# Optimization experiments

Hardware: AMD Instinct MI355X
Metric: run time of the kernel (lower is better)

Reference implementation:

```python
import jax, jax.numpy as jnp
from jax import lax
import numpy as np

B, L, D = 8, 2048, 512
Q, K = 8, 2048


def setup_inputs() -> dict:
    key = jax.random.key(0)
    kx, kc = jax.random.split(key)
    x = jax.random.normal(kx, (B, L, D), dtype=jnp.float32)
    codebooks = jax.random.normal(kc, (Q, K, D), dtype=jnp.float32)  # Q stacked [K, D] embedding tables
    return {"x": x, "codebooks": codebooks}


def reference(x, codebooks):
    # Residual VQ: at each level, nearest-codeword lookup on the residual.
    # cdist argmin == squared-distance argmin: ||r||^2 - 2 r.c + ||c||^2.
    cb_sq = jnp.sum(codebooks * codebooks, axis=-1)  # [Q, K]

    def step(residual, level):
        cb, cb2 = level  # [K, D], [K]
        r2 = jnp.sum(residual * residual, axis=-1, keepdims=True)  # [B, L, 1]
        dots = jnp.einsum('bld,kd->blk', residual, cb)  # [B, L, K]
        dist2 = r2 - 2.0 * dots + cb2  # [B, L, K]
        idx = jnp.argmin(dist2, axis=-1)  # [B, L]
        quant = cb[idx]  # [B, L, D] gather
        return residual - quant, (idx, quant)

    _, (indices, quants) = lax.scan(step, x, (codebooks, cb_sq))
    quantized = jnp.sum(quants, axis=0)  # [B, L, D]
    indices = jnp.moveaxis(indices, 0, 1)  # [B, Q, L] (torch.stack(dim=1))
    return indices, quantized
```

## Files before the change

### kernel.cpp

```cpp
#include <hip/hip_runtime.h>

#define BB 8
#define LL 2048
#define DD 512
#define QQ 8
#define KK 2048
#define MM (BB*LL)

#define NTILES 16

typedef __attribute__((ext_vector_type(8))) short short8;
typedef __attribute__((ext_vector_type(4))) float f32x4;

#define GLDS(src, dst) __builtin_amdgcn_global_load_lds( \
    (const __attribute__((address_space(1))) void*)(src), \
    (__attribute__((address_space(3))) void*)(dst), 16, 0, 0)

#define BARX()  asm volatile("s_barrier" ::: "memory")
#define WAIT0() asm volatile("s_waitcnt vmcnt(0)" ::: "memory")

__device__ __forceinline__ ushort f2bf(float f) {
    uint u = __float_as_uint(f);
    u += 0x7FFFu + ((u >> 16) & 1u);
    return (ushort)(u >> 16);
}

__global__ __launch_bounds__(256) void bprep_kernel(const float* __restrict__ cb,
                                                    short8* __restrict__ bh2all,
                                                    float* __restrict__ cb2) {
    const int wid  = threadIdx.x >> 6;
    const int lane = threadIdx.x & 63;
    const int col  = blockIdx.x * 4 + wid;
    const float* src = cb + (size_t)col * DD + lane * 8;
    float4 v0 = *(const float4*)src;
    float4 v1 = *(const float4*)(src + 4);
    short8 h;
    h[0] = (short)f2bf(v0.x); h[1] = (short)f2bf(v0.y);
    h[2] = (short)f2bf(v0.z); h[3] = (short)f2bf(v0.w);
    h[4] = (short)f2bf(v1.x); h[5] = (short)f2bf(v1.y);
    h[6] = (short)f2bf(v1.z); h[7] = (short)f2bf(v1.w);
    bh2all[(size_t)col * 64 + lane] = h;
    float s = v0.x*v0.x + v0.y*v0.y + v0.z*v0.z + v0.w*v0.w
            + v1.x*v1.x + v1.y*v1.y + v1.z*v1.z + v1.w*v1.w;
    #pragma unroll
    for (int off = 32; off >= 1; off >>= 1) s += __shfl_xor(s, off);
    if (lane == 0) cb2[col] = s;
}

__global__ __launch_bounds__(256) void aprep0_kernel(const float* __restrict__ x,
                                                     float* __restrict__ resid,
                                                     short8* __restrict__ ah) {
    const int wid  = threadIdx.x >> 6;
    const int lane = threadIdx.x & 63;
    const int row  = blockIdx.x * 4 + wid;
    const float* src = x + (size_t)row * DD + lane * 8;
    float4 v0 = *(const float4*)src;
    float4 v1 = *(const float4*)(src + 4);
    float* dst = resid + (size_t)row * DD + lane * 8;
    *(float4*)dst       = v0;
    *(float4*)(dst + 4) = v1;
    short8 h;
    h[0] = (short)f2bf(v0.x); h[1] = (short)f2bf(v0.y);
    h[2] = (short)f2bf(v0.z); h[3] = (short)f2bf(v0.w);
    h[4] = (short)f2bf(v1.x); h[5] = (short)f2bf(v1.y);
    h[6] = (short)f2bf(v1.z); h[7] = (short)f2bf(v1.w);
    ah[(size_t)row * 64 + lane] = h;
}

__global__ __launch_bounds__(512, 2) void gemm_argmin_kernel(
    const short8* __restrict__ ah,
    const short8* __restrict__ bh2q,
    const float*  __restrict__ cb2q,
    float*        __restrict__ blockv1,
    uint4*        __restrict__ blockmask,
    float W)
{
    __shared__ char smemc[131072];

    const int id  = blockIdx.x;
    const int xcd = id & 7;
    const int s   = id >> 3;
    const int nt  = s & 7;
    const int mt  = xcd * 8 + (s >> 3);

    const int tid  = threadIdx.x;
    const int wid  = tid >> 6;
    const int lane = tid & 63;
    const int wr   = wid >> 2;
    const int wcn  = wid & 3;
    const int l15  = lane & 15, l4 = lane >> 4;

    f32x4 acc[4][8];
    #pragma unroll
    for (int n = 0; n < 4; n++)
        #pragma unroll
        for (int m = 0; m < 8; m++) acc[n][m] = (f32x4){0.f, 0.f, 0.f, 0.f};

    const char* aSrc = (const char*)ah   + ((size_t)mt << 18);
    const char* bSrc = (const char*)bh2q + ((size_t)nt << 18);

    #define STAGEQ(tt, bufn, p) do { \
        int g_ = (p) * 512 + tid; \
        int rL_ = g_ >> 3, st_ = g_ & 7; \
        int k_ = st_ ^ (rL_ & 7); \
        char* db_ = smemc + (bufn) * 65536 + ((p) * 512 + wid * 64) * 16; \
        GLDS(aSrc + (size_t)rL_ * 1024 + (tt) * 128 + k_ * 16, db_); \
        GLDS(bSrc + (size_t)rL_ * 1024 + (tt) * 128 + k_ * 16, db_ + 32768); \
    } while (0)

    short8 af[4][2], bf[4][2];

    #define LDA(mh) do { \
        _Pragma("unroll") for (int mm = 0; mm < 4; mm++) \
        _Pragma("unroll") for (int ks = 0; ks < 2; ks++) { \
            int rL_ = wr * 128 + ((mh) * 4 + mm) * 16 + l15; \
            int c_ = ks * 4 + l4; \
            af[mm][ks] = *(const short8*)(smemc + ab + rL_ * 128 + ((c_ ^ (rL_ & 7)) << 4)); \
        } } while (0)

    #define LDBALL() do { \
        _Pragma("unroll") for (int nn = 0; nn < 4; nn++) \
        _Pragma("unroll") for (int ks = 0; ks < 2; ks++) { \
            int cL_ = wcn * 64 + nn * 16 + l15; \
            int c_ = ks * 4 + l4; \
            bf[nn][ks] = *(const short8*)(smemc + ab + 32768 + cL_ * 128 + ((c_ ^ (cL_ & 7)) << 4)); \
        } } while (0)

    #define PH(mh) do { \
        __builtin_amdgcn_s_setprio(1); \
        _Pragma("unroll") for (int ks = 0; ks < 2; ks++) \
        _Pragma("unroll") for (int nn = 0; nn < 4; nn++) \
        _Pragma("unroll") for (int mm = 0; mm < 4; mm++) \
            acc[nn][(mh)*4+mm] = __builtin_amdgcn_mfma_f32_16x16x32_bf16( \
                bf[nn][ks], af[mm][ks], acc[nn][(mh)*4+mm], 0, 0, 0); \
        __builtin_amdgcn_s_setprio(0); \
    } while (0)

    STAGEQ(0, 0, 0); STAGEQ(0, 0, 1); STAGEQ(0, 0, 2); STAGEQ(0, 0, 3);
    WAIT0();
    BARX();

    for (int t = 0; t < 8; t++) {
        const uint ab = (uint)(t & 1) * 65536u;
        const int nbuf = (t & 1) ^ 1;
        if (t < 7) { STAGEQ(t + 1, nbuf, 0); STAGEQ(t + 1, nbuf, 1);
                     STAGEQ(t + 1, nbuf, 2); STAGEQ(t + 1, nbuf, 3); }
        LDBALL();
        LDA(0);
        PH(0);
        LDA(1);
        PH(1);
        if (t < 7) WAIT0();
        BARX();
    }

    float* halfmin = (float*)smemc;
    uint2* maskS   = (uint2*)(smemc + 4096);

    f32x4 c2v[4];
    #pragma unroll
    for (int n = 0; n < 4; n++)
        c2v[n] = *(const f32x4*)&cb2q[nt * 256 + wcn * 64 + n * 16 + (l4 << 2)];

    #pragma unroll
    for (int m = 0; m < 8; m++) {
        float v = 3.4e38f;
        #pragma unroll
        for (int n = 0; n < 4; n++)
            #pragma unroll
            for (int r = 0; r < 4; r++)
                v = fminf(v, fmaf(-2.f, acc[n][m][r], c2v[n][r]));
        v = fminf(v, __shfl_xor(v, 16));
        v = fminf(v, __shfl_xor(v, 32));
        if (l4 == 0) halfmin[(wr * 128 + m * 16 + l15) * 4 + wcn] = v;
    }
    __syncthreads();

    #pragma unroll
    for (int m = 0; m < 8; m++) {
        int rL = wr * 128 + m * 16 + l15;
        int pb = wcn & 2;
        float vt = fminf(halfmin[rL * 4 + pb], halfmin[rL * 4 + pb + 1]);
        float thrm = vt + W;
        uint blo = 0, bhi = 0;
        #pragma unroll
        for (int n = 0; n < 4; n++)
            #pragma unroll
            for (int r = 0; r < 4; r++) {
                float d = fmaf(-2.f, acc[n][m][r], c2v[n][r]);
                int bit = n * 16 + (l4 << 2) + r;
                if (d < thrm) { if (bit < 32) blo |= 1u << bit; else bhi |= 1u << (bit - 32); }
            }
        blo |= __shfl_xor(blo, 16); bhi |= __shfl_xor(bhi, 16);
        blo |= __shfl_xor(blo, 32); bhi |= __shfl_xor(bhi, 32);
        if (l4 == 0) maskS[rL * 4 + wcn] = make_uint2(blo, bhi);
    }
    __syncthreads();

    {
        int T = tid >> 8, rL = tid & 255;
        float vt = fminf(halfmin[rL * 4 + T * 2], halfmin[rL * 4 + T * 2 + 1]);
        uint2 lo = maskS[rL * 4 + T * 2], hi = maskS[rL * 4 + T * 2 + 1];
        size_t o = (size_t)(nt * 2 + T) * MM + mt * 256 + rL;
        blockv1[o] = vt;
        blockmask[o] = make_uint4(lo.x, lo.y, hi.x, hi.y);
    }
    #undef STAGEQ
    #undef LDA
    #undef LDBALL
    #undef PH
}

__global__ __launch_bounds__(256) void crru_kernel(
    const float*  __restrict__ blockv1,
    const uint4*  __restrict__ blockmask,
    const float*  __restrict__ cbq,
    const float*  __restrict__ cb2q,
    const float*  __restrict__ xin,
    float*        __restrict__ resid,
    float*        __restrict__ idx_out,
    short8*       __restrict__ ah,
    int q, float W)
{
    __shared__ float rs[4][DD];
    const int wid  = threadIdx.x >> 6;
    const int lane = threadIdx.x & 63;
    const int row  = blockIdx.x * 4 + wid;
    const int grp  = lane >> 4, gl = lane & 15;

    float v1 = 3.4e38f;
    uint4 mk = make_uint4(0, 0, 0, 0);
    if (lane < NTILES) {
        size_t o = (size_t)lane * MM + row;
        v1 = blockv1[o];
        mk = blockmask[o];
    }

    float* rrow = resid + (size_t)row * DD + lane * 8;
    float4 r0 = *(const float4*)rrow;
    float4 r1 = *(const float4*)(rrow + 4);
    *(float4*)&rs[wid][lane * 8]     = r0;
    *(float4*)&rs[wid][lane * 8 + 4] = r1;

    float g1 = v1;
    #pragma unroll
    for (int off = 32; off >= 1; off >>= 1) g1 = fminf(g1, __shfl_xor(g1, off));
    const float thr = g1 + W;

    unsigned long long act = __ballot((lane < NTILES) && (v1 < thr));

    float be = 3.4e38f; int bk = 0x7FFFFFFF;
    const float* rsw = rs[wid];

    auto eval4 = [&](int k0, int k1, int k2, int k3) {
        int kg = (grp == 0) ? k0 : (grp == 1) ? k1 : (grp == 2) ? k2 : k3;
        float d = 0.f;
        if (kg >= 0) {
            const float* cp = cbq + (size_t)kg * DD + gl * 32;
            const float* rp = rsw + gl * 32;
            #pragma unroll
            for (int j = 0; j < 8; j++) {
                float4 c = *(const float4*)(cp + j * 4);
                float4 r = *(const float4*)(rp + j * 4);
                d = fmaf(r.x, c.x, d); d = fmaf(r.y, c.y, d);
                d = fmaf(r.z, c.z, d); d = fmaf(r.w, c.w, d);
            }
        }
        #pragma unroll
        for (int off = 8; off >= 1; off >>= 1) d += __shfl_xor(d, off);
        #pragma unroll
        for (int g = 0; g < 4; g++) {
            float dg = __shfl(d, g * 16);
            int kg2 = (g == 0) ? k0 : (g == 1) ? k1 : (g == 2) ? k2 : k3;
            if (kg2 >= 0) {
                float e = fmaf(-2.f, dg, cb2q[kg2]);
                if (e < be || (e == be && kg2 < bk)) { be = e; bk = kg2; }
            }
        }
    };

    while (act) {
        int tile = __ffsll(act) - 1; act &= act - 1;
        uint m0 = __shfl((int)mk.x, tile), m1 = __shfl((int)mk.y, tile);
        uint m2 = __shfl((int)mk.z, tile), m3 = __shfl((int)mk.w, tile);
        unsigned long long lo = ((unsigned long long)m1 << 32) | m0;
        unsigned long long hi = ((unsigned long long)m3 << 32) | m2;
        int base = tile * 128;
        while (lo | hi) {
            int c0 = -1, c1 = -1, c2 = -1, c3 = -1;
            #define POP1(dst) \
                if (lo) { int b = __ffsll(lo) - 1; lo &= lo - 1; dst = base + b; } \
                else if (hi) { int b = __ffsll(hi) - 1; hi &= hi - 1; dst = base + 64 + b; }
            POP1(c0) POP1(c1) POP1(c2) POP1(c3)
            #undef POP1
            eval4(c0, c1, c2, c3);
        }
    }
    const int winner = bk;

    if (lane == 0) {
        int b = row >> 11, l = row & (LL - 1);
        idx_out[((size_t)b * QQ + q) * LL + l] = (float)winner;
    }

    const float* cw = cbq + (size_t)winner * DD + lane * 8;
    float4 c0 = *(const float4*)cw;
    float4 c1 = *(const float4*)(cw + 4);
    float4 n0 = make_float4(r0.x - c0.x, r0.y - c0.y, r0.z - c0.z, r0.w - c0.w);
    float4 n1 = make_float4(r1.x - c1.x, r1.y - c1.y, r1.z - c1.z, r1.w - c1.w);

    if (q < QQ - 1) {
        *(float4*)rrow       = n0;
        *(float4*)(rrow + 4) = n1;
        short8 h;
        h[0] = (short)f2bf(n0.x); h[1] = (short)f2bf(n0.y);
        h[2] = (short)f2bf(n0.z); h[3] = (short)f2bf(n0.w);
        h[4] = (short)f2bf(n1.x); h[5] = (short)f2bf(n1.y);
        h[6] = (short)f2bf(n1.z); h[7] = (short)f2bf(n1.w);
        ah[(size_t)row * 64 + lane] = h;
    } else {
        const float* xw = xin + (size_t)row * DD + lane * 8;
        float4 x0 = *(const float4*)xw;
        float4 x1 = *(const float4*)(xw + 4);
        *(float4*)rrow       = make_float4(x0.x - n0.x, x0.y - n0.y, x0.z - n0.z, x0.w - n0.w);
        *(float4*)(rrow + 4) = make_float4(x1.x - n1.x, x1.y - n1.y, x1.z - n1.z, x1.w - n1.w);
    }
}

extern "C" void kernel_launch(void* const* d_in, const int* in_sizes, int n_in,
                              void* d_out, int out_size, void* d_ws, size_t ws_size,
                              hipStream_t stream) {
    (void)in_sizes; (void)n_in; (void)out_size; (void)ws_size;
    const float* x  = (const float*)d_in[0];
    const float* cb = (const float*)d_in[1];
    float* out = (float*)d_out;

    float* idx_out = out;
    float* resid   = out + (size_t)BB * QQ * LL;

    char* w = (char*)d_ws;
    float*  cb2       = (float*)(w);
    float*  blockv1   = (float*)(w + 0x10000);
    uint4*  blockmask = (uint4*)(w + 0x110000);
    short8* ah        = (short8*)(w + 0x510000);
    short8* bh2all    = (short8*)(w + 0x1510000);

    bprep_kernel<<<QQ * KK / 4, 256, 0, stream>>>(cb, bh2all, cb2);
    aprep0_kernel<<<MM / 4, 256, 0, stream>>>(x, resid, ah);

    for (int q = 0; q < QQ; q++) {
        const float* cbq  = cb + (size_t)q * KK * DD;
        const float* c2q  = cb2 + (size_t)q * KK;
        const short8* bhq = bh2all + (size_t)q * KK * 64;
        const float W = 2.0f + 0.3f * q;

        gemm_argmin_kernel<<<512, 512, 0, stream>>>(ah, bhq, c2q,
                                                    blockv1, blockmask, W);

        crru_kernel<<<MM / 4, 256, 0, stream>>>(blockv1, blockmask, cbq, c2q, x,
                                                resid, idx_out, ah, q, W);
    }
}
```

Measured before the change: 500.1 us.

## Split GEMM K-tile into half-stages with partial vmcnt waits and interleaved A/B LDS layout

The bf16 MFMA distance GEMM now stages each K-tile in two halves, each holding interleaved A and B rows under a new swizzle, instead of four quarter-copies of A and B. The main loop waits with vmcnt(4) rather than draining all loads. Barriers move so the copy of the next tile's half starts right after the current half is consumed. The aim is to overlap global-to-LDS copies with MFMA work at finer grain and remove full vmcnt(0) stalls, at the cost of more barriers per tile and a more complex swizzle that must stay correct.

```diff
diff --git a/kernel.cpp b/kernel.cpp
--- a/kernel.cpp
+++ b/kernel.cpp
@@ -16,8 +16,9 @@
     (const __attribute__((address_space(1))) void*)(src), \
     (__attribute__((address_space(3))) void*)(dst), 16, 0, 0)
 
-#define BARX()  asm volatile("s_barrier" ::: "memory")
-#define WAIT0() asm volatile("s_waitcnt vmcnt(0)" ::: "memory")
+#define BARX()   asm volatile("s_barrier" ::: "memory")
+#define WAIT0()  asm volatile("s_waitcnt vmcnt(0)" ::: "memory")
+#define WAITV4() asm volatile("s_waitcnt vmcnt(4)" ::: "memory")
 
 __device__ __forceinline__ ushort f2bf(float f) {
     uint u = __float_as_uint(f);
@@ -99,59 +100,57 @@
     const char* aSrc = (const char*)ah   + ((size_t)mt << 18);
     const char* bSrc = (const char*)bh2q + ((size_t)nt << 18);
 
-    #define STAGEQ(tt, bufn, p) do { \
-        int g_ = (p) * 512 + tid; \
-        int rL_ = g_ >> 3, st_ = g_ & 7; \
-        int k_ = st_ ^ (rL_ & 7); \
-        char* db_ = smemc + (bufn) * 65536 + ((p) * 512 + wid * 64) * 16; \
-        GLDS(aSrc + (size_t)rL_ * 1024 + (tt) * 128 + k_ * 16, db_); \
-        GLDS(bSrc + (size_t)rL_ * 1024 + (tt) * 128 + k_ * 16, db_ + 32768); \
-    } while (0)
-
-    short8 af[4][2], bf[4][2];
-
-    #define LDA(mh) do { \
-        _Pragma("unroll") for (int mm = 0; mm < 4; mm++) \
-        _Pragma("unroll") for (int ks = 0; ks < 2; ks++) { \
-            int rL_ = wr * 128 + ((mh) * 4 + mm) * 16 + l15; \
-            int c_ = ks * 4 + l4; \
-            af[mm][ks] = *(const short8*)(smemc + ab + rL_ * 128 + ((c_ ^ (rL_ & 7)) << 4)); \
+    #define STAGEH(tt, bufn, h) do { \
+        _Pragma("unroll") for (int j = 0; j < 4; j++) { \
+            int g_  = wid * 4 + j; \
+            int pr_ = g_ * 8 + (lane >> 3); \
+            int isB_ = ((lane >> 2) & 1) ^ ((pr_ >> 2) & 1); \
+            int sl_  = (lane & 3) ^ (pr_ & 3); \
+            const char* s_ = (isB_ ? bSrc : aSrc) + (size_t)pr_ * 1024 \
+                             + (tt) * 128 + ((h) * 4 + sl_) * 16; \
+            GLDS(s_, smemc + (bufn) * 65536 + (h) * 32768 + g_ * 1024); \
         } } while (0)
 
-    #define LDBALL() do { \
+    short8 af[8], bf[4];
+
+    #define LDAB(ks) do { \
+        _Pragma("unroll") for (int mm = 0; mm < 8; mm++) { \
+            int rL_ = wr * 128 + mm * 16 + l15; \
+            af[mm] = *(const short8*)(smemc + ab + (ks) * 32768 + rL_ * 128 \
+                     + (((rL_ >> 2) & 1) << 6) + ((l4 ^ (rL_ & 3)) << 4)); \
+        } \
+        _Pragma("unroll") for (int nn = 0; nn < 4; nn++) { \
+            int cL_ = wcn * 64 + nn * 16 + l15; \
+            bf[nn] = *(const short8*)(smemc + ab + (ks) * 32768 + cL_ * 128 \
+                     + ((1 ^ ((cL_ >> 2) & 1)) << 6) + ((l4 ^ (cL_ & 3)) << 4)); \
+        } } while (0)
+
+    #define PHALL() do { \
+        __builtin_amdgcn_s_setprio(1); \
         _Pragma("unroll") for (int nn = 0; nn < 4; nn++) \
-        _Pragma("unroll") for (int ks = 0; ks < 2; ks++) { \
-            int cL_ = wcn * 64 + nn * 16 + l15; \
-            int c_ = ks * 4 + l4; \
-            bf[nn][ks] = *(const short8*)(smemc + ab + 32768 + cL_ * 128 + ((c_ ^ (cL_ & 7)) << 4)); \
-        } } while (0)
-
-    #define PH(mh) do { \
-        __builtin_amdgcn_s_setprio(1); \
-        _Pragma("unroll") for (int ks = 0; ks < 2; ks++) \
-        _Pragma("unroll") for (int nn = 0; nn < 4; nn++) \
-        _Pragma("unroll") for (int mm = 0; mm < 4; mm++) \
-            acc[nn][(mh)*4+mm] = __builtin_amdgcn_mfma_f32_16x16x32_bf16( \
-                bf[nn][ks], af[mm][ks], acc[nn][(mh)*4+mm], 0, 0, 0); \
+        _Pragma("unroll") for (int mm = 0; mm < 8; mm++) \
+            acc[nn][mm] = __builtin_amdgcn_mfma_f32_16x16x32_bf16( \
+                bf[nn], af[mm], acc[nn][mm], 0, 0, 0); \
         __builtin_amdgcn_s_setprio(0); \
     } while (0)
 
-    STAGEQ(0, 0, 0); STAGEQ(0, 0, 1); STAGEQ(0, 0, 2); STAGEQ(0, 0, 3);
-    WAIT0();
-    BARX();
-
+    STAGEH(0, 0, 0);
+    STAGEH(0, 0, 1);
+
+    #pragma unroll
     for (int t = 0; t < 8; t++) {
         const uint ab = (uint)(t & 1) * 65536u;
         const int nbuf = (t & 1) ^ 1;
-        if (t < 7) { STAGEQ(t + 1, nbuf, 0); STAGEQ(t + 1, nbuf, 1);
-                     STAGEQ(t + 1, nbuf, 2); STAGEQ(t + 1, nbuf, 3); }
-        LDBALL();
-        LDA(0);
-        PH(0);
-        LDA(1);
-        PH(1);
-        if (t < 7) WAIT0();
+        WAITV4();
         BARX();
+        if (t < 7) STAGEH(t + 1, nbuf, 0);
+        LDAB(0);
+        PHALL();
+        if (t < 7) { WAITV4(); } else { WAIT0(); }
+        BARX();
+        if (t < 7) STAGEH(t + 1, nbuf, 1);
+        LDAB(1);
+        PHALL();
     }
 
     float* halfmin = (float*)smemc;
@@ -205,10 +204,9 @@
         blockv1[o] = vt;
         blockmask[o] = make_uint4(lo.x, lo.y, hi.x, hi.y);
     }
-    #undef STAGEQ
-    #undef LDA
-    #undef LDBALL
-    #undef PH
+    #undef STAGEH
+    #undef LDAB
+    #undef PHALL
 }
 
 __global__ __launch_bounds__(256) void crru_kernel(
```

New measurement: 504.7 us. Within noise of the previous version (+0.9%).

## Split GEMM tile loads into quarter stages with partial vmcnt waits

Applied to the files above, without the earlier changes.

The bf16 MFMA distance GEMM loop is restructured from whole-tile double buffering with a full vmcnt(0) wait per k-step into four quarter-tile stages. Each stage covers A or B rows for one half of the wave's subtile. Compute on each quarter starts after only its own data has landed (vmcnt(4)/vmcnt(2)) and loads for the next k-tile are issued in between, so global-to-LDS traffic overlaps more with MFMA work. The cost is more barriers per iteration, harder index math for the staging, and the risk of getting the wait-count or buffer ordering wrong.

```diff
diff --git a/kernel.cpp b/kernel.cpp
--- a/kernel.cpp
+++ b/kernel.cpp
@@ -16,8 +16,10 @@
     (const __attribute__((address_space(1))) void*)(src), \
     (__attribute__((address_space(3))) void*)(dst), 16, 0, 0)
 
-#define BARX()  asm volatile("s_barrier" ::: "memory")
-#define WAIT0() asm volatile("s_waitcnt vmcnt(0)" ::: "memory")
+#define BARX()   asm volatile("s_barrier" ::: "memory")
+#define WAIT0()  asm volatile("s_waitcnt vmcnt(0)" ::: "memory")
+#define WAITV2() asm volatile("s_waitcnt vmcnt(2)" ::: "memory")
+#define WAITV4() asm volatile("s_waitcnt vmcnt(4)" ::: "memory")
 
 __device__ __forceinline__ ushort f2bf(float f) {
     uint u = __float_as_uint(f);
@@ -99,14 +101,20 @@
     const char* aSrc = (const char*)ah   + ((size_t)mt << 18);
     const char* bSrc = (const char*)bh2q + ((size_t)nt << 18);
 
-    #define STAGEQ(tt, bufn, p) do { \
-        int g_ = (p) * 512 + tid; \
-        int rL_ = g_ >> 3, st_ = g_ & 7; \
-        int k_ = st_ ^ (rL_ & 7); \
-        char* db_ = smemc + (bufn) * 65536 + ((p) * 512 + wid * 64) * 16; \
-        GLDS(aSrc + (size_t)rL_ * 1024 + (tt) * 128 + k_ * 16, db_); \
-        GLDS(bSrc + (size_t)rL_ * 1024 + (tt) * 128 + k_ * 16, db_ + 32768); \
-    } while (0)
+    #define STAGEU(tt, bufn, isB, u) do { \
+        _Pragma("unroll") for (int j = 0; j < 2; j++) { \
+            int riu0 = j * 64 + wid * 8;                 \
+            int riu  = riu0 + (lane >> 3); \
+            int st   = lane & 7; \
+            int rc  = (isB) ? (((riu  >> 5) << 6) + (u) * 32 + (riu  & 31)) \
+                            : (((riu  >> 6) << 7) + (u) * 64 + (riu  & 63)); \
+            int rc0 = (isB) ? (((riu0 >> 5) << 6) + (u) * 32 + (riu0 & 31)) \
+                            : (((riu0 >> 6) << 7) + (u) * 64 + (riu0 & 63)); \
+            int k_ = st ^ (rc & 7); \
+            const char* s_ = ((isB) ? bSrc : aSrc) + (size_t)rc * 1024 \
+                             + (tt) * 128 + k_ * 16; \
+            GLDS(s_, smemc + (bufn) * 65536 + ((isB) ? 32768 : 0) + rc0 * 128); \
+        } } while (0)
 
     short8 af[4][2], bf[4][2];
 
@@ -118,40 +126,60 @@
             af[mm][ks] = *(const short8*)(smemc + ab + rL_ * 128 + ((c_ ^ (rL_ & 7)) << 4)); \
         } } while (0)
 
-    #define LDBALL() do { \
-        _Pragma("unroll") for (int nn = 0; nn < 4; nn++) \
+    #define LDB2(nh) do { \
+        _Pragma("unroll") for (int n2 = 0; n2 < 2; n2++) \
         _Pragma("unroll") for (int ks = 0; ks < 2; ks++) { \
+            int nn = (nh) * 2 + n2; \
             int cL_ = wcn * 64 + nn * 16 + l15; \
             int c_ = ks * 4 + l4; \
             bf[nn][ks] = *(const short8*)(smemc + ab + 32768 + cL_ * 128 + ((c_ ^ (cL_ & 7)) << 4)); \
         } } while (0)
 
-    #define PH(mh) do { \
+    #define PHQ(mh, nh) do { \
         __builtin_amdgcn_s_setprio(1); \
         _Pragma("unroll") for (int ks = 0; ks < 2; ks++) \
-        _Pragma("unroll") for (int nn = 0; nn < 4; nn++) \
+        _Pragma("unroll") for (int n2 = 0; n2 < 2; n2++) \
         _Pragma("unroll") for (int mm = 0; mm < 4; mm++) \
-            acc[nn][(mh)*4+mm] = __builtin_amdgcn_mfma_f32_16x16x32_bf16( \
-                bf[nn][ks], af[mm][ks], acc[nn][(mh)*4+mm], 0, 0, 0); \
+            acc[(nh)*2+n2][(mh)*4+mm] = __builtin_amdgcn_mfma_f32_16x16x32_bf16( \
+                bf[(nh)*2+n2][ks], af[mm][ks], acc[(nh)*2+n2][(mh)*4+mm], 0, 0, 0); \
         __builtin_amdgcn_s_setprio(0); \
     } while (0)
 
-    STAGEQ(0, 0, 0); STAGEQ(0, 0, 1); STAGEQ(0, 0, 2); STAGEQ(0, 0, 3);
-    WAIT0();
-    BARX();
-
-    for (int t = 0; t < 8; t++) {
+    STAGEU(0, 0, 0, 0);
+    STAGEU(0, 0, 1, 0);
+    STAGEU(0, 0, 1, 1);
+    STAGEU(0, 0, 0, 1);
+
+    for (int t = 0; t < 7; t++) {
         const uint ab = (uint)(t & 1) * 65536u;
         const int nbuf = (t & 1) ^ 1;
-        if (t < 7) { STAGEQ(t + 1, nbuf, 0); STAGEQ(t + 1, nbuf, 1);
-                     STAGEQ(t + 1, nbuf, 2); STAGEQ(t + 1, nbuf, 3); }
-        LDBALL();
-        LDA(0);
-        PH(0);
+        WAITV4(); BARX();
+        STAGEU(t + 1, nbuf, 0, 0);
+        LDA(0); LDB2(0);
+        PHQ(0, 0);
+        WAITV4(); BARX();
+        STAGEU(t + 1, nbuf, 1, 0);
+        LDB2(1);
+        PHQ(0, 1);
+        WAITV4(); BARX();
+        STAGEU(t + 1, nbuf, 1, 1);
         LDA(1);
-        PH(1);
-        if (t < 7) WAIT0();
-        BARX();
+        PHQ(1, 0);
+        STAGEU(t + 1, nbuf, 0, 1);
+        PHQ(1, 1);
+    }
+    {
+        const uint ab = 65536u;
+        WAITV4(); BARX();
+        LDA(0); LDB2(0);
+        PHQ(0, 0);
+        WAITV2(); BARX();
+        LDB2(1);
+        PHQ(0, 1);
+        WAIT0(); BARX();
+        LDA(1);
+        PHQ(1, 0);
+        PHQ(1, 1);
     }
 
     float* halfmin = (float*)smemc;
@@ -205,10 +233,10 @@
         blockv1[o] = vt;
         blockmask[o] = make_uint4(lo.x, lo.y, hi.x, hi.y);
     }
-    #undef STAGEQ
+    #undef STAGEU
     #undef LDA
-    #undef LDBALL
-    #undef PH
+    #undef LDB2
+    #undef PHQ
 }
 
 __global__ __launch_bounds__(256) void crru_kernel(
```

Result: faster. 489.2 us (-2.2%).
